# Kernel tuning notes

Measured on AMD Instinct MI355X. Metric: run time of the kernel, lower is better.

The kernel has to match this reference:

```python
import jax, jax.numpy as jnp
import numpy as np

SR = 16000.0
WIN = 400
SHIFT = 160
NMEL = 80
PREEMPH = 0.97
EPS = float(np.finfo(np.float64).eps)


def _mel_banks(num_bins, win, sr):
    # kaldi-compatible triangular mel banks, low_freq=20, high_freq=nyquist
    def hz2mel(f):
        return 1127.0 * np.log(1.0 + f / 700.0)
    mlow, mhigh = hz2mel(20.0), hz2mel(sr / 2.0)
    d = (mhigh - mlow) / (num_bins + 1)
    left = mlow + np.arange(num_bins) * d
    center = left + d
    right = left + 2 * d
    fft_freqs = (sr / win) * np.arange(win // 2)
    mel = hz2mel(fft_freqs)[None, :]
    up = (mel - left[:, None]) / d
    down = (right[:, None] - mel) / d
    banks = np.maximum(0.0, np.minimum(up, down))
    banks = np.concatenate([banks, np.zeros((num_bins, 1))], axis=1)  # pad last rfft bin
    return jnp.asarray(banks, jnp.float32)

_BANKS = _mel_banks(NMEL, WIN, SR)
_WINDOW = jnp.asarray(0.5 - 0.5 * np.cos(2 * np.pi * np.arange(WIN) / (WIN - 1)), jnp.float32)


def setup_inputs() -> dict:
    key = jax.random.key(0)
    k1, k2 = jax.random.split(key)
    B, L = 64, 240000
    x = jax.random.normal(k1, (B, L), dtype=jnp.float32)
    T = jax.random.randint(k2, (B,), 1, L, dtype=jnp.int32)
    normalizer = jnp.full((NMEL,), 0.1, dtype=jnp.float32)  # Parameter init 1/10
    return {"x": x, "T": T, "normalizer": normalizer}


def _fbank(x, normalizer):
    B, L = x.shape
    n_frames = 1 + (L - WIN) // SHIFT  # snip_edges=True
    idx = np.arange(n_frames)[:, None] * SHIFT + np.arange(WIN)[None, :]
    frames = x[:, idx]
    # preemphasis: frame[i] -= 0.97 * frame[i-1]; first sample uses itself
    prev = jnp.concatenate([frames[..., :1], frames[..., :-1]], axis=-1)
    frames = (frames - PREEMPH * prev) * _WINDOW
    spec = jnp.abs(jnp.fft.rfft(frames, axis=-1)) ** 2
    mel = jnp.einsum('bfk,mk->bfm', spec, _BANKS)
    mel = jnp.log(jnp.maximum(mel, EPS))
    return mel * normalizer[None, None, :]


def reference(x, T, normalizer):
    fb = _fbank(x, normalizer)                            # (B, F, M)
    B, F, M = fb.shape
    # faithful to source: downsample_factor = max(T) / fbanks[0].shape[1] (= num_mel_bins)
    ds = jnp.max(T).astype(jnp.float32) / M
    T_ = (T.astype(jnp.float32) / ds).astype(jnp.int32)   # int() truncation, T >= 0
    mask = (jnp.arange(F)[None, :] < T_[:, None])[..., None]  # (B, F, 1)
    cnt = jnp.maximum(T_, 1).astype(fb.dtype)[:, None, None]
    mean = jnp.sum(jnp.where(mask, fb, 0.0), axis=1, keepdims=True) / cnt
    return jnp.where(mask, fb - mean, fb)
```

## Files before the change

kernel.cpp:

```cpp
#include <hip/hip_runtime.h>
#include <hip/hip_bf16.h>

#define BATCH   64
#define LSIG    240000
#define WIN     400
#define SHIFT   160
#define NFR     1498
#define NMEL    80
#define NBIN    200
#define NF      8
#define MAXW    14
#define SPECW   (NBIN + MAXW)

#define SSTR    44
#define SFR     (11 * SSTR)
#define S_TOT   (NF * SFR)
#define WIN_OFF  S_TOT
#define TW1_OFF (S_TOT + 400)
#define XSEG_OFF (S_TOT + 840)
#define SPEC_OFF S_TOT
#define LDS_TOT (S_TOT + 840 + 1520)

__global__ __launch_bounds__(256, 6)
void fbank_kernel(const float* __restrict__ x, const float* __restrict__ norm,
                  float* __restrict__ out) {
    const int ft = blockIdx.x;
    const int b  = blockIdx.y;
    const int f0 = ft * NF;
    const int nf = min(NF, NFR - f0);
    const int tid = threadIdx.x;

    __shared__ __align__(16) float smem[LDS_TOT];
    float* Sb   = smem;
    float* winS = smem + WIN_OFF;
    float* tw1S = smem + TW1_OFF;
    float* xseg = smem + XSEG_OFF;
    float* spec = smem + SPEC_OFF;

    const float TWO_PI = 6.2831853071795864769f;

    const float* xb = x + (size_t)b * LSIG + (size_t)f0 * SHIFT;
    const int seglen = (nf - 1) * SHIFT + WIN;
    for (int i = tid; i < seglen; i += 256) xseg[i] = xb[i];

    for (int j = tid; j < WIN; j += 256)
        winS[j] = 0.5f - 0.5f * __cosf(TWO_PI * (float)j / 399.0f);
    for (int i = tid; i < 220; i += 256) {
        int r = i / 20, t1 = i - r * 20;
        int j = (r * t1 * 20) % 400;
        float th = (float)j * (-TWO_PI / 400.0f);
        tw1S[2 * i]     = __cosf(th);
        tw1S[2 * i + 1] = __sinf(th);
    }
    __syncthreads();

    if (tid < nf * 20) {
        const int f = tid / 20, t2 = tid - f * 20;
        const float* xf = xseg + f * SHIFT;
        float yr[20];
#pragma unroll
        for (int t1 = 0; t1 < 20; t1++) {
            int t = t2 + 20 * t1;
            float xc = xf[t];
            float xp = xf[t > 0 ? t - 1 : 0];
            yr[t1] = (xc - 0.97f * xp) * winS[t];
        }
        float* Sf = Sb + f * SFR + t2 * 2;
#pragma unroll
        for (int r = 0; r <= 10; r++) {
            float ar = 0.0f, ai = 0.0f;
#pragma unroll
            for (int t1 = 0; t1 < 20; t1++) {
                float2 cs = *(const float2*)(tw1S + 2 * (r * 20 + t1));
                ar = fmaf(yr[t1], cs.x, ar);
                ai = fmaf(yr[t1], cs.y, ai);
            }
            *(float2*)(Sf + r * SSTR) = make_float2(ar, ai);
        }
    }
    __syncthreads();

    {
        const int k = tid;
        if (k < NBIN) {
            int r = k % 20;
            int rp   = (r > 10) ? 20 - r : r;
            float sg = (r > 10) ? -1.0f : 1.0f;
            float twc[20], tws[20];
#pragma unroll
            for (int t2 = 0; t2 < 20; t2++) {
                int j = (k * t2) % 400;
                float th = (float)j * (-TWO_PI / 400.0f);
                twc[t2] = __cosf(th);
                tws[t2] = __sinf(th) * sg;
            }
            for (int f = 0; f < nf; f++) {
                const float4* Sf = (const float4*)(Sb + f * SFR + rp * SSTR);
                float xr0 = 0.f, xi0 = 0.f, xr1 = 0.f, xi1 = 0.f;
#pragma unroll
                for (int q = 0; q < 10; q++) {
                    float4 v = Sf[q];
                    float c0 = twc[2 * q],     s0 = tws[2 * q];
                    float c1 = twc[2 * q + 1], s1 = tws[2 * q + 1];
                    xr0 = fmaf(c0, v.x, fmaf(-s0, v.y, xr0));
                    xi0 = fmaf(s0, v.x, fmaf(c0,  v.y, xi0));
                    xr1 = fmaf(c1, v.z, fmaf(-s1, v.w, xr1));
                    xi1 = fmaf(s1, v.z, fmaf(c1,  v.w, xi1));
                }
                float xr = xr0 + xr1, xi = xi0 + xi1;
                spec[f * SPECW + k] = fmaf(xr, xr, xi * xi);
            }
        } else if (k < SPECW) {
            for (int f = 0; f < NF; f++) spec[f * SPECW + k] = 0.0f;
        }
    }
    __syncthreads();

    if (tid < 240) {
        const int m = tid % 80;
        const int g = tid / 80;
        const float mlow  = 1127.0f * __logf(1.0f + 20.0f / 700.0f);
        const float mhigh = 1127.0f * __logf(1.0f + 8000.0f / 700.0f);
        const float d     = (mhigh - mlow) * (1.0f / 81.0f);
        const float left  = mlow + (float)m * d;
        const float inv_d = 1.0f / d;
        float freq_left = 700.0f * (__expf(left * (1.0f / 1127.0f)) - 1.0f);
        int kstart = (int)floorf(freq_left * 0.025f) + 1;
        float w[MAXW];
#pragma unroll
        for (int j = 0; j < MAXW; j++) {
            float melk = 1127.0f * __logf(1.0f + (float)(kstart + j) * (40.0f / 700.0f));
            float up = (melk - left) * inv_d;
            float dn = 2.0f - up;
            w[j] = fmaxf(0.0f, fminf(up, dn));
        }
        const float nm = norm[m];
        for (int i = 0; i < 3; i++) {
            int f = g + 3 * i;
            if (f < nf) {
                const float* sp = spec + f * SPECW + kstart;
                float acc = 0.0f;
#pragma unroll
                for (int j = 0; j < MAXW; j++)
                    acc = fmaf(w[j], sp[j], acc);
                float mel = fmaxf(acc, 2.2204460492503131e-16f);
                out[((size_t)b * NFR + (f0 + f)) * NMEL + m] = __logf(mel) * nm;
            }
        }
    }
}

__global__ __launch_bounds__(256)
void meansub_kernel(float* __restrict__ out, const int* __restrict__ T) {
    const int b = blockIdx.x;
    __shared__ float part[3][NMEL];
    __shared__ float meanSh[NMEL];

    int maxT = T[0];
    for (int i = 1; i < BATCH; i++) maxT = max(maxT, T[i]);
    float ds = (float)maxT / (float)NMEL;
    int tb = (int)((float)T[b] / ds);

    const int q = threadIdx.x / NMEL;
    const int m = threadIdx.x - q * NMEL;
    float* pb = out + (size_t)b * NFR * NMEL;

    if (q < 3) {
        float s = 0.0f;
        for (int f = q; f < tb; f += 3) s += pb[(size_t)f * NMEL + m];
        part[q][m] = s;
    }
    __syncthreads();
    if (threadIdx.x < NMEL)
        meanSh[m] = (part[0][m] + part[1][m] + part[2][m]) / (float)max(tb, 1);
    __syncthreads();
    if (q < 3) {
        float mean = meanSh[m];
        for (int f = q; f < tb; f += 3) pb[(size_t)f * NMEL + m] -= mean;
    }
}

extern "C" void kernel_launch(void* const* d_in, const int* in_sizes, int n_in,
                              void* d_out, int out_size, void* d_ws, size_t ws_size,
                              hipStream_t stream) {
    const float* x    = (const float*)d_in[0];
    const int*   T    = (const int*)d_in[1];
    const float* norm = (const float*)d_in[2];
    float* out = (float*)d_out;

    dim3 grid((NFR + NF - 1) / NF, BATCH);
    fbank_kernel<<<grid, 256, 0, stream>>>(x, norm, out);

    meansub_kernel<<<BATCH, 256, 0, stream>>>(out, T);
}
```

Before: 230.9 us.

## Use compile-time twiddles and pair conjugate bins across frames in DFT stages

The first DFT stage now uses twiddle constants computed at compile time through templates. Multiplications by 0 and ±1 are elided, and the shared-memory twiddle table and its setup loop are gone. The second stage is reorganised so each thread computes bins k and 20-k together for four frames. Each loaded float4 of stage-1 output is reused across both bins, and twiddles come from a precomputed constant global table instead of per-thread sincos. In exchange, twiddle traffic moves from sincos math to global/cache loads, and the per-thread register footprint grows.

New measurement: 207.2 us. 1.11x faster.

```diff
diff --git a/kernel.cpp b/kernel.cpp
--- a/kernel.cpp
+++ b/kernel.cpp
@@ -1,5 +1,4 @@
 #include <hip/hip_runtime.h>
-#include <hip/hip_bf16.h>
 
 #define BATCH   64
 #define LSIG    240000
@@ -16,10 +15,64 @@
 #define SFR     (11 * SSTR)
 #define S_TOT   (NF * SFR)
 #define WIN_OFF  S_TOT
-#define TW1_OFF (S_TOT + 400)
-#define XSEG_OFF (S_TOT + 840)
+#define XSEG_OFF (S_TOT + WIN)
 #define SPEC_OFF S_TOT
-#define LDS_TOT (S_TOT + 840 + 1520)
+#define LDS_TOT (S_TOT + WIN + 1520)
+
+constexpr double D_PI = 3.14159265358979323846264338327950288;
+constexpr double tsin(double x){ double x2=x*x,t=x,s=x; for(int n=1;n<=13;++n){ t*=-x2/double((2*n)*(2*n+1)); s+=t;} return s; }
+constexpr double tcos(double x){ double x2=x*x,t=1.0,s=1.0; for(int n=1;n<=13;++n){ t*=-x2/double((2*n-1)*(2*n)); s+=t;} return s; }
+constexpr float cos400(int j){ int a=((j%400)+400)%400; int q=a/100, rem=a%100; double x=D_PI*(double)rem/200.0;
+    double v = q==0? tcos(x) : q==1? -tsin(x) : q==2? -tcos(x) : tsin(x); return (float)v; }
+constexpr float sin400(int j){ int a=((j%400)+400)%400; int q=a/100, rem=a%100; double x=D_PI*(double)rem/200.0;
+    double v = q==0? tsin(x) : q==1? tcos(x) : q==2? -tsin(x) : -tcos(x); return (float)v; }
+
+struct Tw2Tab {
+    float v[10][110][8];
+    constexpr Tw2Tab() : v{} {
+        for (int q=0;q<10;++q) for (int u=0;u<110;++u) {
+            int m=u/11, rp=u%11;
+            int k1 = rp + 20*m;
+            bool val2 = (rp>=1 && rp<=9);
+            int k2 = val2 ? (20-rp+20*m) : k1;
+            int ta=2*q, tb=2*q+1;
+            v[q][u][0] = cos400(k1*ta); v[q][u][1] = -sin400(k1*ta);
+            v[q][u][2] = cos400(k1*tb); v[q][u][3] = -sin400(k1*tb);
+            v[q][u][4] = cos400(k2*ta); v[q][u][5] = val2 ?  sin400(k2*ta) : -sin400(k2*ta);
+            v[q][u][6] = cos400(k2*tb); v[q][u][7] = val2 ?  sin400(k2*tb) : -sin400(k2*tb);
+        }
+    }
+};
+__device__ const Tw2Tab g_tw2{};
+
+template<int R, int T1> struct Mac1 {
+    static __device__ __forceinline__ void go(const float* yr, float& ar, float& ai) {
+        constexpr int j = ((R * T1) % 20) * 20;
+        constexpr float c = cos400(j);
+        constexpr float s = -sin400(j);
+        float y = yr[T1];
+        if constexpr (c == 1.0f)       ar += y;
+        else if constexpr (c == -1.0f) ar -= y;
+        else if constexpr (c == 0.0f)  {}
+        else                           ar = fmaf(y, c, ar);
+        if constexpr (s == 1.0f)       ai += y;
+        else if constexpr (s == -1.0f) ai -= y;
+        else if constexpr (s == 0.0f)  {}
+        else                           ai = fmaf(y, s, ai);
+        Mac1<R, T1 + 1>::go(yr, ar, ai);
+    }
+};
+template<int R> struct Mac1<R, 20> { static __device__ __forceinline__ void go(const float*, float&, float&) {} };
+
+template<int R> struct Dft1 {
+    static __device__ __forceinline__ void go(const float* yr, float* Sf) {
+        float ar = 0.0f, ai = 0.0f;
+        Mac1<R, 0>::go(yr, ar, ai);
+        *(float2*)(Sf + R * SSTR) = make_float2(ar, ai);
+        Dft1<R + 1>::go(yr, Sf);
+    }
+};
+template<> struct Dft1<11> { static __device__ __forceinline__ void go(const float*, float*) {} };
 
 __global__ __launch_bounds__(256, 6)
 void fbank_kernel(const float* __restrict__ x, const float* __restrict__ norm,
@@ -33,25 +86,15 @@
     __shared__ __align__(16) float smem[LDS_TOT];
     float* Sb   = smem;
     float* winS = smem + WIN_OFF;
-    float* tw1S = smem + TW1_OFF;
     float* xseg = smem + XSEG_OFF;
     float* spec = smem + SPEC_OFF;
-
-    const float TWO_PI = 6.2831853071795864769f;
 
     const float* xb = x + (size_t)b * LSIG + (size_t)f0 * SHIFT;
     const int seglen = (nf - 1) * SHIFT + WIN;
     for (int i = tid; i < seglen; i += 256) xseg[i] = xb[i];
-
+    const float TWO_PI = 6.28318530717958647693f;
     for (int j = tid; j < WIN; j += 256)
         winS[j] = 0.5f - 0.5f * __cosf(TWO_PI * (float)j / 399.0f);
-    for (int i = tid; i < 220; i += 256) {
-        int r = i / 20, t1 = i - r * 20;
-        int j = (r * t1 * 20) % 400;
-        float th = (float)j * (-TWO_PI / 400.0f);
-        tw1S[2 * i]     = __cosf(th);
-        tw1S[2 * i + 1] = __sinf(th);
-    }
     __syncthreads();
 
     if (tid < nf * 20) {
@@ -59,60 +102,54 @@
         const float* xf = xseg + f * SHIFT;
         float yr[20];
 #pragma unroll
-        for (int t1 = 0; t1 < 20; t1++) {
+        for (int t1 = 0; t1 < 20; ++t1) {
             int t = t2 + 20 * t1;
             float xc = xf[t];
             float xp = xf[t > 0 ? t - 1 : 0];
             yr[t1] = (xc - 0.97f * xp) * winS[t];
         }
-        float* Sf = Sb + f * SFR + t2 * 2;
-#pragma unroll
-        for (int r = 0; r <= 10; r++) {
-            float ar = 0.0f, ai = 0.0f;
-#pragma unroll
-            for (int t1 = 0; t1 < 20; t1++) {
-                float2 cs = *(const float2*)(tw1S + 2 * (r * 20 + t1));
-                ar = fmaf(yr[t1], cs.x, ar);
-                ai = fmaf(yr[t1], cs.y, ai);
+        Dft1<0>::go(yr, Sb + f * SFR + 2 * t2);
+    }
+    __syncthreads();
+
+    if (tid < 220) {
+        const int fhalf = tid / 110, u = tid - fhalf * 110;
+        const int m = u / 11, rp = u - m * 11;
+        const int k1 = rp + 20 * m;
+        const int k2 = 20 - rp + 20 * m;
+        const bool valid2 = (rp >= 1 && rp <= 9);
+        float xr1[4], xi1[4], xr2[4], xi2[4];
+#pragma unroll
+        for (int fi = 0; fi < 4; ++fi) { xr1[fi]=0.f; xi1[fi]=0.f; xr2[fi]=0.f; xi2[fi]=0.f; }
+        const float* Sbase = Sb + (fhalf * 4) * SFR + rp * SSTR;
+#pragma unroll 2
+        for (int q = 0; q < 10; ++q) {
+            const float4 ta = *(const float4*)&g_tw2.v[q][u][0];
+            const float4 tb = *(const float4*)&g_tw2.v[q][u][4];
+#pragma unroll
+            for (int fi = 0; fi < 4; ++fi) {
+                float4 v = *(const float4*)(Sbase + fi * SFR + 4 * q);
+                xr1[fi] = fmaf(ta.x, v.x, xr1[fi]); xr1[fi] = fmaf(-ta.y, v.y, xr1[fi]);
+                xi1[fi] = fmaf(ta.y, v.x, xi1[fi]); xi1[fi] = fmaf( ta.x, v.y, xi1[fi]);
+                xr1[fi] = fmaf(ta.z, v.z, xr1[fi]); xr1[fi] = fmaf(-ta.w, v.w, xr1[fi]);
+                xi1[fi] = fmaf(ta.w, v.z, xi1[fi]); xi1[fi] = fmaf( ta.z, v.w, xi1[fi]);
+                xr2[fi] = fmaf(tb.x, v.x, xr2[fi]); xr2[fi] = fmaf(-tb.y, v.y, xr2[fi]);
+                xi2[fi] = fmaf(tb.y, v.x, xi2[fi]); xi2[fi] = fmaf( tb.x, v.y, xi2[fi]);
+                xr2[fi] = fmaf(tb.z, v.z, xr2[fi]); xr2[fi] = fmaf(-tb.w, v.w, xr2[fi]);
+                xi2[fi] = fmaf(tb.w, v.z, xi2[fi]); xi2[fi] = fmaf( tb.z, v.w, xi2[fi]);
             }
-            *(float2*)(Sf + r * SSTR) = make_float2(ar, ai);
-        }
-    }
-    __syncthreads();
-
-    {
-        const int k = tid;
-        if (k < NBIN) {
-            int r = k % 20;
-            int rp   = (r > 10) ? 20 - r : r;
-            float sg = (r > 10) ? -1.0f : 1.0f;
-            float twc[20], tws[20];
-#pragma unroll
-            for (int t2 = 0; t2 < 20; t2++) {
-                int j = (k * t2) % 400;
-                float th = (float)j * (-TWO_PI / 400.0f);
-                twc[t2] = __cosf(th);
-                tws[t2] = __sinf(th) * sg;
-            }
-            for (int f = 0; f < nf; f++) {
-                const float4* Sf = (const float4*)(Sb + f * SFR + rp * SSTR);
-                float xr0 = 0.f, xi0 = 0.f, xr1 = 0.f, xi1 = 0.f;
-#pragma unroll
-                for (int q = 0; q < 10; q++) {
-                    float4 v = Sf[q];
-                    float c0 = twc[2 * q],     s0 = tws[2 * q];
-                    float c1 = twc[2 * q + 1], s1 = tws[2 * q + 1];
-                    xr0 = fmaf(c0, v.x, fmaf(-s0, v.y, xr0));
-                    xi0 = fmaf(s0, v.x, fmaf(c0,  v.y, xi0));
-                    xr1 = fmaf(c1, v.z, fmaf(-s1, v.w, xr1));
-                    xi1 = fmaf(s1, v.z, fmaf(c1,  v.w, xi1));
-                }
-                float xr = xr0 + xr1, xi = xi0 + xi1;
-                spec[f * SPECW + k] = fmaf(xr, xr, xi * xi);
-            }
-        } else if (k < SPECW) {
-            for (int f = 0; f < NF; f++) spec[f * SPECW + k] = 0.0f;
-        }
+        }
+#pragma unroll
+        for (int fi = 0; fi < 4; ++fi) {
+            int f = fhalf * 4 + fi;
+            spec[f * SPECW + k1] = fmaf(xr1[fi], xr1[fi], xi1[fi] * xi1[fi]);
+            if (valid2)
+                spec[f * SPECW + k2] = fmaf(xr2[fi], xr2[fi], xi2[fi] * xi2[fi]);
+        }
+    } else if (tid < 220 + MAXW) {
+        const int kp = NBIN + (tid - 220);
+#pragma unroll
+        for (int f = 0; f < NF; ++f) spec[f * SPECW + kp] = 0.0f;
     }
     __syncthreads();
 
```

## Restructure DFT stages with compile-time twiddles and radix-4 second stage

Applied to the files above, without the earlier changes.

Stage one of the 400-point DFT now uses compile-time twiddle constants through template recursion, skipping trivial multiplies by 0 and ±1. The window moves into per-thread registers instead of LDS. Stage two is split into a 5x4 radix-style decomposition that produces four output bins per thread, using a precomputed constexpr twiddle table in device global memory. This is meant to cut the FMA count and LDS traffic of the naive 20-point DFT per bin, at the cost of more complex code and register pressure.

Result: faster. 202.5 us (-12.3%).

```diff
diff --git a/kernel.cpp b/kernel.cpp
--- a/kernel.cpp
+++ b/kernel.cpp
@@ -1,5 +1,4 @@
 #include <hip/hip_runtime.h>
-#include <hip/hip_bf16.h>
 
 #define BATCH   64
 #define LSIG    240000
@@ -13,13 +12,72 @@
 #define SPECW   (NBIN + MAXW)
 
 #define SSTR    44
-#define SFR     (11 * SSTR)
+#define SFR     484
 #define S_TOT   (NF * SFR)
-#define WIN_OFF  S_TOT
-#define TW1_OFF (S_TOT + 400)
-#define XSEG_OFF (S_TOT + 840)
+#define XSEG_OFF S_TOT
 #define SPEC_OFF S_TOT
-#define LDS_TOT (S_TOT + 840 + 1520)
+#define LDS_TOT (S_TOT + NF * SPECW)
+
+constexpr double D_PI = 3.14159265358979323846264338327950288;
+constexpr double tsin(double x){ double x2=x*x,t=x,s=x; for(int n=1;n<=13;++n){ t*=-x2/double((2*n)*(2*n+1)); s+=t;} return s; }
+constexpr double tcos(double x){ double x2=x*x,t=1.0,s=1.0; for(int n=1;n<=13;++n){ t*=-x2/double((2*n-1)*(2*n)); s+=t;} return s; }
+constexpr float cos400(int j){ int a=((j%400)+400)%400; int q=a/100, rem=a%100; double x=D_PI*(double)rem/200.0;
+    double v = q==0? tcos(x) : q==1? -tsin(x) : q==2? -tcos(x) : tsin(x); return (float)v; }
+constexpr float sin400(int j){ int a=((j%400)+400)%400; int q=a/100, rem=a%100; double x=D_PI*(double)rem/200.0;
+    double v = q==0? tsin(x) : q==1? tcos(x) : q==2? -tsin(x) : -tcos(x); return (float)v; }
+
+struct Tw3 {
+    float v[55][32];
+    constexpr Tw3() : v{} {
+        for (int m5=0;m5<5;++m5) for (int rp=0;rp<11;++rp) {
+            int u = m5*11+rp;
+            int k1 = rp + 20*m5;
+            int k2 = (20-rp) + 20*m5;
+            for (int tb=1; tb<=4; ++tb) {
+                v[u][2*(tb-1)]     =  cos400(4*k1*tb);
+                v[u][2*(tb-1)+1]   = -sin400(4*k1*tb);
+                v[u][8+2*(tb-1)]   =  cos400(4*k2*tb);
+                v[u][8+2*(tb-1)+1] = -sin400(4*k2*tb);
+            }
+            for (int ta=1; ta<=3; ++ta) {
+                v[u][16+2*(ta-1)]   =  cos400(k1*ta);
+                v[u][16+2*(ta-1)+1] = -sin400(k1*ta);
+                v[u][22+2*(ta-1)]   =  cos400(k2*ta);
+                v[u][22+2*(ta-1)+1] = -sin400(k2*ta);
+            }
+        }
+    }
+};
+__device__ const Tw3 g_tw3{};
+
+template<int T1, int R> struct Mac1R {
+    static __device__ __forceinline__ void go(float y, float* ar, float* ai) {
+        constexpr int j = ((R * T1) % 20) * 20;
+        constexpr float c =  cos400(j);
+        constexpr float s = -sin400(j);
+        if constexpr (c == 1.0f)       ar[R] += y;
+        else if constexpr (c == -1.0f) ar[R] -= y;
+        else if constexpr (c != 0.0f)  ar[R] = fmaf(y, c, ar[R]);
+        if constexpr (s == 1.0f)       ai[R] += y;
+        else if constexpr (s == -1.0f) ai[R] -= y;
+        else if constexpr (s != 0.0f)  ai[R] = fmaf(y, s, ai[R]);
+        Mac1R<T1, R + 1>::go(y, ar, ai);
+    }
+};
+template<int T1> struct Mac1R<T1, 11> { static __device__ __forceinline__ void go(float, float*, float*) {} };
+
+template<int T1> struct Col {
+    static __device__ __forceinline__ void go(const float* xf, int t2, const float* wreg,
+                                              float* ar, float* ai) {
+        int t = t2 + 20 * T1;
+        int tp = t - 1;
+        if constexpr (T1 == 0) tp = max(tp, 0);
+        float y = (xf[t] - 0.97f * xf[tp]) * wreg[T1];
+        Mac1R<T1, 0>::go(y, ar, ai);
+        Col<T1 + 1>::go(xf, t2, wreg, ar, ai);
+    }
+};
+template<> struct Col<20> { static __device__ __forceinline__ void go(const float*, int, const float*, float*, float*) {} };
 
 __global__ __launch_bounds__(256, 6)
 void fbank_kernel(const float* __restrict__ x, const float* __restrict__ norm,
@@ -32,87 +90,120 @@
 
     __shared__ __align__(16) float smem[LDS_TOT];
     float* Sb   = smem;
-    float* winS = smem + WIN_OFF;
-    float* tw1S = smem + TW1_OFF;
     float* xseg = smem + XSEG_OFF;
     float* spec = smem + SPEC_OFF;
-
-    const float TWO_PI = 6.2831853071795864769f;
 
     const float* xb = x + (size_t)b * LSIG + (size_t)f0 * SHIFT;
     const int seglen = (nf - 1) * SHIFT + WIN;
     for (int i = tid; i < seglen; i += 256) xseg[i] = xb[i];
 
-    for (int j = tid; j < WIN; j += 256)
-        winS[j] = 0.5f - 0.5f * __cosf(TWO_PI * (float)j / 399.0f);
-    for (int i = tid; i < 220; i += 256) {
-        int r = i / 20, t1 = i - r * 20;
-        int j = (r * t1 * 20) % 400;
-        float th = (float)j * (-TWO_PI / 400.0f);
-        tw1S[2 * i]     = __cosf(th);
-        tw1S[2 * i + 1] = __sinf(th);
+    const float TWO_PI = 6.28318530717958647693f;
+    float wreg[20];
+    {
+        const int t2w = tid % 20;
+#pragma unroll
+        for (int t1 = 0; t1 < 20; ++t1)
+            wreg[t1] = 0.5f - 0.5f * __cosf(TWO_PI * (float)(t2w + 20 * t1) / 399.0f);
     }
     __syncthreads();
 
     if (tid < nf * 20) {
         const int f = tid / 20, t2 = tid - f * 20;
-        const float* xf = xseg + f * SHIFT;
-        float yr[20];
-#pragma unroll
-        for (int t1 = 0; t1 < 20; t1++) {
-            int t = t2 + 20 * t1;
-            float xc = xf[t];
-            float xp = xf[t > 0 ? t - 1 : 0];
-            yr[t1] = (xc - 0.97f * xp) * winS[t];
-        }
-        float* Sf = Sb + f * SFR + t2 * 2;
-#pragma unroll
-        for (int r = 0; r <= 10; r++) {
-            float ar = 0.0f, ai = 0.0f;
-#pragma unroll
-            for (int t1 = 0; t1 < 20; t1++) {
-                float2 cs = *(const float2*)(tw1S + 2 * (r * 20 + t1));
-                ar = fmaf(yr[t1], cs.x, ar);
-                ai = fmaf(yr[t1], cs.y, ai);
-            }
-            *(float2*)(Sf + r * SSTR) = make_float2(ar, ai);
-        }
-    }
-    __syncthreads();
-
-    {
-        const int k = tid;
-        if (k < NBIN) {
-            int r = k % 20;
-            int rp   = (r > 10) ? 20 - r : r;
-            float sg = (r > 10) ? -1.0f : 1.0f;
-            float twc[20], tws[20];
-#pragma unroll
-            for (int t2 = 0; t2 < 20; t2++) {
-                int j = (k * t2) % 400;
-                float th = (float)j * (-TWO_PI / 400.0f);
-                twc[t2] = __cosf(th);
-                tws[t2] = __sinf(th) * sg;
-            }
-            for (int f = 0; f < nf; f++) {
-                const float4* Sf = (const float4*)(Sb + f * SFR + rp * SSTR);
-                float xr0 = 0.f, xi0 = 0.f, xr1 = 0.f, xi1 = 0.f;
-#pragma unroll
-                for (int q = 0; q < 10; q++) {
-                    float4 v = Sf[q];
-                    float c0 = twc[2 * q],     s0 = tws[2 * q];
-                    float c1 = twc[2 * q + 1], s1 = tws[2 * q + 1];
-                    xr0 = fmaf(c0, v.x, fmaf(-s0, v.y, xr0));
-                    xi0 = fmaf(s0, v.x, fmaf(c0,  v.y, xi0));
-                    xr1 = fmaf(c1, v.z, fmaf(-s1, v.w, xr1));
-                    xi1 = fmaf(s1, v.z, fmaf(c1,  v.w, xi1));
+        float ar[11], ai[11];
+#pragma unroll
+        for (int r = 0; r < 11; ++r) { ar[r] = 0.0f; ai[r] = 0.0f; }
+        Col<0>::go(xseg + f * SHIFT, t2, wreg, ar, ai);
+        float* Sf = Sb + f * SFR + 2 * t2;
+#pragma unroll
+        for (int r = 0; r < 11; ++r)
+            *(float2*)(Sf + r * SSTR) = make_float2(ar[r], ai[r]);
+    }
+    __syncthreads();
+
+    if (tid < 220) {
+        const int fquad = tid / 55, u = tid - fquad * 55;
+        const int m5 = u / 11, rp = u - m5 * 11;
+        const int k1 = rp + 20 * m5;
+        const int k2 = (20 - rp) + 20 * m5;
+        const bool valid2 = (rp >= 1 && rp <= 9);
+
+        const float4* tp4 = (const float4*)&g_tw3.v[u][0];
+        float4 w0 = tp4[0], w1 = tp4[1], w2 = tp4[2], w3 = tp4[3];
+        float4 w4 = tp4[4], w5 = tp4[5], w6 = tp4[6];
+        float t1c[5], t1s[5], t2c[5], t2s[5];
+        t1c[1]=w0.x; t1s[1]=w0.y; t1c[2]=w0.z; t1s[2]=w0.w;
+        t1c[3]=w1.x; t1s[3]=w1.y; t1c[4]=w1.z; t1s[4]=w1.w;
+        t2c[1]=w2.x; t2s[1]=w2.y; t2c[2]=w2.z; t2s[2]=w2.w;
+        t2c[3]=w3.x; t2s[3]=w3.y; t2c[4]=w3.z; t2s[4]=w3.w;
+        float b1c[4], b1s[4], b2c[4], b2s[4];
+        b1c[1]=w4.x; b1s[1]=w4.y; b1c[2]=w4.z; b1s[2]=w4.w;
+        b1c[3]=w5.x; b1s[3]=w5.y;
+        b2c[1]=w5.z; b2s[1]=w5.w; b2c[2]=w6.x; b2s[2]=w6.y;
+        b2c[3]=w6.z; b2s[3]=w6.w;
+
+#pragma unroll
+        for (int fi = 0; fi < 2; ++fi) {
+            const int f = 2 * fquad + fi;
+            if (f < nf) {
+                const float* Sf = Sb + f * SFR + rp * SSTR;
+                float4 v0 = *(const float4*)(Sf);
+                float4 v1 = *(const float4*)(Sf + 4);
+                float U1r[4], U1i[4], U2r[4], U2i[4];
+                U1r[0]=v0.x; U1i[0]=v0.y; U2r[0]=v0.x; U2i[0]=-v0.y;
+                U1r[1]=v0.z; U1i[1]=v0.w; U2r[1]=v0.z; U2i[1]=-v0.w;
+                U1r[2]=v1.x; U1i[2]=v1.y; U2r[2]=v1.x; U2i[2]=-v1.y;
+                U1r[3]=v1.z; U1i[3]=v1.w; U2r[3]=v1.z; U2i[3]=-v1.w;
+#pragma unroll
+                for (int q = 2; q < 10; ++q) {
+                    float4 v = *(const float4*)(Sf + 4 * q);
+                    const int tb = q >> 1;
+                    const int ta = (q & 1) * 2;
+                    float c = t1c[tb], s = t1s[tb], c2 = t2c[tb], s2 = t2s[tb];
+                    U1r[ta]   = fmaf(c,  v.x, fmaf(-s,  v.y, U1r[ta]));
+                    U1i[ta]   = fmaf(s,  v.x, fmaf( c,  v.y, U1i[ta]));
+                    U2r[ta]   = fmaf(c2, v.x, fmaf( s2, v.y, U2r[ta]));
+                    U2i[ta]   = fmaf(s2, v.x, fmaf(-c2, v.y, U2i[ta]));
+                    U1r[ta+1] = fmaf(c,  v.z, fmaf(-s,  v.w, U1r[ta+1]));
+                    U1i[ta+1] = fmaf(s,  v.z, fmaf( c,  v.w, U1i[ta+1]));
+                    U2r[ta+1] = fmaf(c2, v.z, fmaf( s2, v.w, U2r[ta+1]));
+                    U2i[ta+1] = fmaf(s2, v.z, fmaf(-c2, v.w, U2i[ta+1]));
                 }
-                float xr = xr0 + xr1, xi = xi0 + xi1;
-                spec[f * SPECW + k] = fmaf(xr, xr, xi * xi);
-            }
-        } else if (k < SPECW) {
-            for (int f = 0; f < NF; f++) spec[f * SPECW + k] = 0.0f;
-        }
+                {
+                    float p1r = fmaf(b1c[1],U1r[1], -b1s[1]*U1i[1]);
+                    float p1i = fmaf(b1s[1],U1r[1],  b1c[1]*U1i[1]);
+                    float p2r = fmaf(b1c[2],U1r[2], -b1s[2]*U1i[2]);
+                    float p2i = fmaf(b1s[2],U1r[2],  b1c[2]*U1i[2]);
+                    float p3r = fmaf(b1c[3],U1r[3], -b1s[3]*U1i[3]);
+                    float p3i = fmaf(b1s[3],U1r[3],  b1c[3]*U1i[3]);
+                    float Xr = (U1r[0] + p1r) + (p2r + p3r);
+                    float Xi = (U1i[0] + p1i) + (p2i + p3i);
+                    float Yr = (U1r[0] + p1i) - (p2r + p3i);
+                    float Yi = (U1i[0] - p1r) + (p3r - p2i);
+                    spec[f * SPECW + k1]       = fmaf(Xr, Xr, Xi * Xi);
+                    spec[f * SPECW + k1 + 100] = fmaf(Yr, Yr, Yi * Yi);
+                }
+                {
+                    float p1r = fmaf(b2c[1],U2r[1], -b2s[1]*U2i[1]);
+                    float p1i = fmaf(b2s[1],U2r[1],  b2c[1]*U2i[1]);
+                    float p2r = fmaf(b2c[2],U2r[2], -b2s[2]*U2i[2]);
+                    float p2i = fmaf(b2s[2],U2r[2],  b2c[2]*U2i[2]);
+                    float p3r = fmaf(b2c[3],U2r[3], -b2s[3]*U2i[3]);
+                    float p3i = fmaf(b2s[3],U2r[3],  b2c[3]*U2i[3]);
+                    float Xr = (U2r[0] + p1r) + (p2r + p3r);
+                    float Xi = (U2i[0] + p1i) + (p2i + p3i);
+                    float Yr = (U2r[0] + p1i) - (p2r + p3i);
+                    float Yi = (U2i[0] - p1r) + (p3r - p2i);
+                    if (valid2) {
+                        spec[f * SPECW + k2]       = fmaf(Xr, Xr, Xi * Xi);
+                        spec[f * SPECW + k2 + 100] = fmaf(Yr, Yr, Yi * Yi);
+                    }
+                }
+            }
+        }
+    } else if (tid < 220 + MAXW) {
+        const int kp = NBIN + (tid - 220);
+#pragma unroll
+        for (int f = 0; f < NF; ++f) spec[f * SPECW + kp] = 0.0f;
     }
     __syncthreads();
 
```
